# Kernel tuning notes

Hardware: AMD Instinct MI355X
Metric: run time of the kernel (lower is better)

## Reference

```python
import jax, jax.numpy as jnp
import numpy as np

B, NNB, D, FF, L = 128, 510, 128, 512, 3
N = NNB + 2  # 2 query tokens (first/last) + neighbors
SQRT_D = float(np.sqrt(D))
LOGIT_CLIP = 10.0
NINF = -1e9


def _layer_norm(x, g, b):
    m = jnp.mean(x, axis=-1, keepdims=True)
    v = jnp.var(x, axis=-1, keepdims=True)
    return (x - m) * jax.lax.rsqrt(v + 1e-5) * g + b


def _aafm(q, k, v, w):
    # Attention-free module: sigmoid(q) * (exp(w) @ (exp(k)*v)) / (exp(w) @ exp(k))
    w = w - jnp.max(w, axis=-1, keepdims=True)          # stable, cancels in ratio
    k = k - jnp.max(k, axis=1, keepdims=True)
    ew = jnp.exp(w)                                      # [B,N,N]
    ek = jnp.exp(k)                                      # [B,N,D]
    num = jnp.einsum('bts,bsd->btd', ew, ek * v)
    den = jnp.einsum('bts,bsd->btd', ew, ek)
    return jax.nn.sigmoid(q) * num / den


def setup_inputs() -> dict:
    key = jax.random.key(0)
    ks = jax.random.split(key, 32)
    s = 1.0 / np.sqrt(D)
    inp = {
        'lower_xy': jax.random.uniform(ks[0], (B, N, 2), jnp.float32),
        'load': jax.random.uniform(ks[1], (B,), jnp.float32) * 0.9 + 0.1,
        'lower_demand': jax.random.uniform(ks[2], (B, NNB, 1), jnp.float32) * 0.3,
        'lower_cur_ninf_mask': jnp.where(
            jax.random.uniform(ks[3], (B, 1, N)) < 0.1, NINF, 0.0).astype(jnp.float32),
        'lower_pairwise_dist': jax.random.uniform(ks[4], (B, N, N), jnp.float32),
        'neighbors_num_list': jnp.full((B,), NNB, dtype=jnp.int32),
        'lower_neighbors_index': jax.random.randint(ks[5], (B, NNB), 0, 100000),
        # learned params (torch Linear stored transposed: here [in, out], y = x @ W)
        'emb_W': jax.random.normal(ks[6], (2, D)) * s,
        'emb_b': jnp.zeros((D,), jnp.float32),
        'w_load': jax.random.normal(ks[7], (D,)) * s,
        'w_demand': jax.random.normal(ks[8], (D,)) * s,
        'Wq_first': jax.random.normal(ks[9], (D, D)) * s,
        'Wq_last': jax.random.normal(ks[10], (D, D)) * s,
        'alpha_com': jnp.ones((1,), jnp.float32),
        'Wq': jax.random.normal(ks[11], (L, D, D)) * s,
        'Wk': jax.random.normal(ks[12], (L, D, D)) * s,
        'Wv': jax.random.normal(ks[13], (L, D, D)) * s,
        'alpha_attn': jnp.ones((L,), jnp.float32),
        'ln1_g': jnp.ones((L, D), jnp.float32),
        'ln1_b': jnp.zeros((L, D), jnp.float32),
        'ln2_g': jnp.ones((L, D), jnp.float32),
        'ln2_b': jnp.zeros((L, D), jnp.float32),
        'ff_W1': jax.random.normal(ks[14], (L, D, FF)) * s,
        'ff_b1': jnp.zeros((L, FF), jnp.float32),
        'ff_W2': jax.random.normal(ks[15], (L, FF, D)) * (1.0 / np.sqrt(FF)),
        'ff_b2': jnp.zeros((L, D), jnp.float32),
    }
    return inp


def reference(lower_xy, load, lower_demand, lower_cur_ninf_mask, lower_pairwise_dist,
              neighbors_num_list, lower_neighbors_index,
              emb_W, emb_b, w_load, w_demand, Wq_first, Wq_last, alpha_com,
              Wq, Wk, Wv, alpha_attn, ln1_g, ln1_b, ln2_g, ln2_b,
              ff_W1, ff_b1, ff_W2, ff_b2):
    load3 = load[:, None, None]                           # [B,1,1]
    load3 = jnp.where(load3 == 0, 1.0, load3)
    fln = lower_xy @ emb_W + emb_b                        # [B,N,D]
    load_emb = load3 * w_load                             # [B,1,D]
    q_first = fln[:, 0:1] @ Wq_first + load_emb
    q_last = fln[:, 1:2] @ Wq_last + load_emb
    demand = jnp.clip(lower_demand / load3, 0.0, 1.0)     # [B,n,1]
    nb = fln[:, 2:] + demand * w_demand                   # [B,n,D]
    nb_mask = lower_cur_ninf_mask[:, 0, 2:]               # [B,n]
    nb = jnp.where((nb_mask < 0)[..., None], 0.0, nb)     # padding overwrite
    x = jnp.concatenate([q_first, q_last, nb], axis=1)    # [B,N,D]

    log_nb = jnp.log2(neighbors_num_list.astype(x.dtype))[:, None, None]
    spd = -log_nb * lower_pairwise_dist                   # [B,N,N]
    mask_full = jnp.broadcast_to(lower_cur_ninf_mask, spd.shape)

    for i in range(L):
        q = x @ Wq[i]; k = x @ Wk[i]; v = x @ Wv[i]
        aafm = _aafm(q, k, v, alpha_attn[i] * spd + mask_full)
        h = _layer_norm(x + aafm, ln1_g[i], ln1_b[i])
        ff = jax.nn.relu(h @ ff_W1[i] + ff_b1[i]) @ ff_W2[i] + ff_b2[i]
        x = _layer_norm(h + ff, ln2_g[i], ln2_b[i])

    q_out = x[:, 0:1] + x[:, 1:2]                         # [B,1,D]
    nbo = x[:, 2:]                                        # [B,n,D]
    bias_com = alpha_com * spd[:, 1, 2:][:, None, :]      # [B,1,n]
    score = jnp.einsum('bqd,bnd->bqn', q_out, nbo) / SQRT_D + bias_com
    score = LOGIT_CLIP * jnp.tanh(score) + lower_cur_ninf_mask[:, :, 2:]
    probs = jax.nn.softmax(score, axis=-1)[:, 0]          # [B,n]

    selected = jnp.argmax(probs, axis=-1)                 # greedy eval
    prob = jnp.take_along_axis(probs, selected[:, None], axis=-1)[:, 0]
    true_selected = jnp.take_along_axis(lower_neighbors_index, selected[:, None], axis=-1)[:, 0]
    return true_selected, prob
```

## Files before the change

### kernel.cpp

```cpp
#include <hip/hip_runtime.h>
#include <math.h>

constexpr int B   = 128;
constexpr int N   = 512;
constexpr int NNB = 510;
constexpr int D   = 128;
constexpr int FFH = 512;
constexpr int NL  = 3;

__device__ __forceinline__ float sigmoidf_(float x) { return 1.f / (1.f + expf(-x)); }

__device__ __forceinline__ float xla_fast_tanh(float x) {
    if (fabsf(x) < 0.0004f) return x;
    const float C = 7.99881172180175781f;
    float xc = fminf(fmaxf(x, -C), C);
    float x2 = __fmul_rn(xc, xc);
    float num = -2.76076847742355e-16f;
    num = __builtin_fmaf(x2, num, 2.00018790482477e-13f);
    num = __builtin_fmaf(x2, num, -8.60467152213735e-11f);
    num = __builtin_fmaf(x2, num, 5.12229709037114e-08f);
    num = __builtin_fmaf(x2, num, 1.48572235717979e-05f);
    num = __builtin_fmaf(x2, num, 6.37261928875436e-04f);
    num = __builtin_fmaf(x2, num, 4.89352455891786e-03f);
    num = __fmul_rn(xc, num);
    float den = 1.19825839466702e-06f;
    den = __builtin_fmaf(x2, den, 1.18534705686654e-04f);
    den = __builtin_fmaf(x2, den, 2.26843463243900e-03f);
    den = __builtin_fmaf(x2, den, 4.89352518554385e-03f);
    return num / den;
}

__global__ __launch_bounds__(128) void build_x_kernel(
    const float* __restrict__ xy, const float* __restrict__ load,
    const float* __restrict__ demand, const float* __restrict__ mask,
    const float* __restrict__ embW, const float* __restrict__ embb,
    const float* __restrict__ wload, const float* __restrict__ wdem,
    const float* __restrict__ Wqf, const float* __restrict__ Wql,
    float* __restrict__ x)
{
    __shared__ float fln[128];
    const int bn = blockIdx.x;
    const int b  = bn >> 9;
    const int n  = bn & 511;
    const int d  = threadIdx.x;
    float l = load[b];
    float load3 = (l == 0.f) ? 1.f : l;

    if (n >= 2) {
        const int j = n - 2;
        float m = mask[(size_t)b * N + n];
        float out = 0.f;
        if (!(m < 0.f)) {
            float x0 = xy[(size_t)bn * 2 + 0];
            float x1 = xy[(size_t)bn * 2 + 1];
            float fl = x0 * embW[d] + x1 * embW[D + d] + embb[d];
            float dm = demand[(size_t)b * NNB + j] / load3;
            dm = fminf(fmaxf(dm, 0.f), 1.f);
            out = fl + dm * wdem[d];
        }
        x[(size_t)bn * D + d] = out;
    } else {
        float x0 = xy[(size_t)bn * 2 + 0];
        float x1 = xy[(size_t)bn * 2 + 1];
        fln[d] = x0 * embW[d] + x1 * embW[D + d] + embb[d];
        __syncthreads();
        const float* W = (n == 0) ? Wqf : Wql;
        float acc = 0.f;
        #pragma unroll 8
        for (int e = 0; e < D; ++e) acc = fmaf(fln[e], W[(size_t)e * D + d], acc);
        x[(size_t)bn * D + d] = acc + load3 * wload[d];
    }
}

template<bool BIAS, bool RELU>
__global__ __launch_bounds__(256) void gemm_f32(
    const float* __restrict__ A, const float* __restrict__ W,
    const float* __restrict__ bias, float* __restrict__ C,
    int M, int K, int Nc)
{
    __shared__ float As[64][40];
    __shared__ float Ws[32][132];
    const int m0 = blockIdx.x * 64;
    const int n0 = blockIdx.y * 128;
    const int tid = threadIdx.x;
    const int tc = tid & 31;
    const int tr = tid >> 5;

    const int ar0 = tid >> 3,          ac0 = (tid & 7) * 4;
    const int ar1 = (tid + 256) >> 3,  ac1 = ((tid + 256) & 7) * 4;
    int wr[4], wc[4];
    #pragma unroll
    for (int i = 0; i < 4; ++i) {
        int f = tid + i * 256;
        wr[i] = f >> 5; wc[i] = (f & 31) * 4;
    }

    float4 acc[8];
    #pragma unroll
    for (int r = 0; r < 8; ++r) acc[r] = make_float4(0.f, 0.f, 0.f, 0.f);

    {
        float4 a0 = *(const float4*)&A[(size_t)(m0 + ar0) * K + ac0];
        float4 a1 = *(const float4*)&A[(size_t)(m0 + ar1) * K + ac1];
        float4 w0 = *(const float4*)&W[(size_t)(0 + wr[0]) * Nc + n0 + wc[0]];
        float4 w1 = *(const float4*)&W[(size_t)(0 + wr[1]) * Nc + n0 + wc[1]];
        float4 w2 = *(const float4*)&W[(size_t)(0 + wr[2]) * Nc + n0 + wc[2]];
        float4 w3 = *(const float4*)&W[(size_t)(0 + wr[3]) * Nc + n0 + wc[3]];
        *(float4*)&As[ar0][ac0] = a0;
        *(float4*)&As[ar1][ac1] = a1;
        *(float4*)&Ws[wr[0]][wc[0]] = w0;
        *(float4*)&Ws[wr[1]][wc[1]] = w1;
        *(float4*)&Ws[wr[2]][wc[2]] = w2;
        *(float4*)&Ws[wr[3]][wc[3]] = w3;
    }
    __syncthreads();

    for (int kt = 0; kt < K; kt += 32) {
        const bool more = (kt + 32) < K;
        float4 na0, na1, nw0, nw1, nw2, nw3;
        if (more) {
            int kn = kt + 32;
            na0 = *(const float4*)&A[(size_t)(m0 + ar0) * K + kn + ac0];
            na1 = *(const float4*)&A[(size_t)(m0 + ar1) * K + kn + ac1];
            nw0 = *(const float4*)&W[(size_t)(kn + wr[0]) * Nc + n0 + wc[0]];
            nw1 = *(const float4*)&W[(size_t)(kn + wr[1]) * Nc + n0 + wc[1]];
            nw2 = *(const float4*)&W[(size_t)(kn + wr[2]) * Nc + n0 + wc[2]];
            nw3 = *(const float4*)&W[(size_t)(kn + wr[3]) * Nc + n0 + wc[3]];
        }
        #pragma unroll
        for (int kk = 0; kk < 32; kk += 4) {
            float4 w0 = *(float4*)&Ws[kk + 0][tc * 4];
            float4 w1 = *(float4*)&Ws[kk + 1][tc * 4];
            float4 w2 = *(float4*)&Ws[kk + 2][tc * 4];
            float4 w3 = *(float4*)&Ws[kk + 3][tc * 4];
            #pragma unroll
            for (int r = 0; r < 8; ++r) {
                float4 a4 = *(float4*)&As[tr * 8 + r][kk];
                acc[r].x = fmaf(a4.x, w0.x, acc[r].x); acc[r].x = fmaf(a4.y, w1.x, acc[r].x);
                acc[r].x = fmaf(a4.z, w2.x, acc[r].x); acc[r].x = fmaf(a4.w, w3.x, acc[r].x);
                acc[r].y = fmaf(a4.x, w0.y, acc[r].y); acc[r].y = fmaf(a4.y, w1.y, acc[r].y);
                acc[r].y = fmaf(a4.z, w2.y, acc[r].y); acc[r].y = fmaf(a4.w, w3.y, acc[r].y);
                acc[r].z = fmaf(a4.x, w0.z, acc[r].z); acc[r].z = fmaf(a4.y, w1.z, acc[r].z);
                acc[r].z = fmaf(a4.z, w2.z, acc[r].z); acc[r].z = fmaf(a4.w, w3.z, acc[r].z);
                acc[r].w = fmaf(a4.x, w0.w, acc[r].w); acc[r].w = fmaf(a4.y, w1.w, acc[r].w);
                acc[r].w = fmaf(a4.z, w2.w, acc[r].w); acc[r].w = fmaf(a4.w, w3.w, acc[r].w);
            }
        }
        if (more) {
            __syncthreads();
            *(float4*)&As[ar0][ac0] = na0;
            *(float4*)&As[ar1][ac1] = na1;
            *(float4*)&Ws[wr[0]][wc[0]] = nw0;
            *(float4*)&Ws[wr[1]][wc[1]] = nw1;
            *(float4*)&Ws[wr[2]][wc[2]] = nw2;
            *(float4*)&Ws[wr[3]][wc[3]] = nw3;
            __syncthreads();
        }
    }

    float4 bv = make_float4(0.f, 0.f, 0.f, 0.f);
    if (BIAS) bv = *(const float4*)&bias[n0 + tc * 4];
    #pragma unroll
    for (int r = 0; r < 8; ++r) {
        float4 o = acc[r];
        if (BIAS) { o.x += bv.x; o.y += bv.y; o.z += bv.z; o.w += bv.w; }
        if (RELU) {
            o.x = fmaxf(o.x, 0.f); o.y = fmaxf(o.y, 0.f);
            o.z = fmaxf(o.z, 0.f); o.w = fmaxf(o.w, 0.f);
        }
        *(float4*)&C[(size_t)(m0 + tr * 8 + r) * Nc + n0 + tc * 4] = o;
    }
}

__global__ __launch_bounds__(128) void colmax_part(
    const float* __restrict__ k, float* __restrict__ part)
{
    int b = blockIdx.x >> 3, c = blockIdx.x & 7, d = threadIdx.x;
    const float* kp = k + ((size_t)b * N + c * 64) * D + d;
    float m = -3.4e38f;
    #pragma unroll 8
    for (int s = 0; s < 64; ++s) m = fmaxf(m, kp[(size_t)s * D]);
    part[(size_t)blockIdx.x * D + d] = m;
}

__global__ __launch_bounds__(128) void ekv_build(
    const float* __restrict__ k, const float* __restrict__ v,
    const float* __restrict__ part, float* __restrict__ ekv)
{
    int b = blockIdx.x >> 3, c = blockIdx.x & 7, d = threadIdx.x;
    float m = -3.4e38f;
    #pragma unroll
    for (int j = 0; j < 8; ++j) m = fmaxf(m, part[((size_t)b * 8 + j) * D + d]);
    for (int s = 0; s < 64; ++s) {
        int sg = c * 64 + s;
        size_t off = ((size_t)b * N + sg) * D + d;
        float ek = expf(k[off] - m);
        size_t o2 = ((size_t)b * N + sg) * 256;
        ekv[o2 + d]       = ek * v[off];
        ekv[o2 + 128 + d] = ek;
    }
}

__global__ __launch_bounds__(256) void attn_kernel(
    const float* __restrict__ pdist, const float* __restrict__ mask,
    const float* __restrict__ ekv, const float* __restrict__ q,
    const int* __restrict__ nnum, const float* __restrict__ alphaAttn, int layer,
    float* __restrict__ att)
{
    __shared__ float ew[16][516];
    __shared__ float red16[16][16];
    __shared__ float rmax[16];
    const int d0  = blockIdx.x;
    const int xcd = d0 & 7;
    const int idx = d0 >> 3;
    const int tl  = idx & 31;
    const int b   = (idx >> 5) * 8 + xcd;
    const int t0  = tl * 16;
    const int tid = threadIdx.x;
    const float la = -log2f((float)nnum[b]) * alphaAttn[layer];
    const float* pd = pdist + ((size_t)b * N + t0) * N;
    const float* mk = mask + (size_t)b * N;

    #pragma unroll
    for (int i = 0; i < 8; ++i) {
        int f = tid + i * 256;
        int r = f >> 7, s4 = (f & 127) * 4;
        float4 p = *(const float4*)&pd[(size_t)r * N + s4];
        float4 m = *(const float4*)&mk[s4];
        float4 w;
        w.x = fmaf(la, p.x, m.x); w.y = fmaf(la, p.y, m.y);
        w.z = fmaf(la, p.z, m.z); w.w = fmaf(la, p.w, m.w);
        *(float4*)&ew[r][s4] = w;
    }
    __syncthreads();
    {
        int r = tid >> 4, j0 = tid & 15;
        float m = -3.4e38f;
        #pragma unroll 8
        for (int j = 0; j < 32; ++j) m = fmaxf(m, ew[r][j0 + 16 * j]);
        red16[r][j0] = m;
    }
    __syncthreads();
    if (tid < 16) {
        float m = red16[tid][0];
        #pragma unroll
        for (int j = 1; j < 16; ++j) m = fmaxf(m, red16[tid][j]);
        rmax[tid] = m;
    }
    __syncthreads();
    #pragma unroll
    for (int i = 0; i < 8; ++i) {
        int f = tid + i * 256;
        int r = f >> 7, s4 = (f & 127) * 4;
        float m = rmax[r];
        float4 w = *(float4*)&ew[r][s4];
        w.x = expf(w.x - m); w.y = expf(w.y - m);
        w.z = expf(w.z - m); w.w = expf(w.w - m);
        *(float4*)&ew[r][s4] = w;
    }
    __syncthreads();

    const int lane = tid & 63;
    const int wv   = tid >> 6;
    const int c4   = lane * 4;
    float4 acc[4];
    #pragma unroll
    for (int r = 0; r < 4; ++r) acc[r] = make_float4(0.f, 0.f, 0.f, 0.f);
    const float* ep = ekv + (size_t)b * N * 256 + c4;
    float4 e0 = *(const float4*)&ep[0 * 256];
    float4 e1 = *(const float4*)&ep[1 * 256];
    float4 e2 = *(const float4*)&ep[2 * 256];
    float4 e3 = *(const float4*)&ep[3 * 256];
    for (int s = 0; s < N; s += 4) {
        float4 f0 = e0, f1 = e1, f2 = e2, f3 = e3;
        int sn = (s + 4 < N) ? (s + 4) : s;
        e0 = *(const float4*)&ep[(size_t)(sn + 0) * 256];
        e1 = *(const float4*)&ep[(size_t)(sn + 1) * 256];
        e2 = *(const float4*)&ep[(size_t)(sn + 2) * 256];
        e3 = *(const float4*)&ep[(size_t)(sn + 3) * 256];
        #pragma unroll
        for (int r = 0; r < 4; ++r) {
            float4 a = *(float4*)&ew[wv * 4 + r][s];
            acc[r].x = fmaf(a.x, f0.x, acc[r].x); acc[r].x = fmaf(a.y, f1.x, acc[r].x);
            acc[r].x = fmaf(a.z, f2.x, acc[r].x); acc[r].x = fmaf(a.w, f3.x, acc[r].x);
            acc[r].y = fmaf(a.x, f0.y, acc[r].y); acc[r].y = fmaf(a.y, f1.y, acc[r].y);
            acc[r].y = fmaf(a.z, f2.y, acc[r].y); acc[r].y = fmaf(a.w, f3.y, acc[r].y);
            acc[r].z = fmaf(a.x, f0.z, acc[r].z); acc[r].z = fmaf(a.y, f1.z, acc[r].z);
            acc[r].z = fmaf(a.z, f2.z, acc[r].z); acc[r].z = fmaf(a.w, f3.z, acc[r].z);
            acc[r].w = fmaf(a.x, f0.w, acc[r].w); acc[r].w = fmaf(a.y, f1.w, acc[r].w);
            acc[r].w = fmaf(a.z, f2.w, acc[r].w); acc[r].w = fmaf(a.w, f3.w, acc[r].w);
        }
    }
    __syncthreads();
    if (c4 >= 128) {
        #pragma unroll
        for (int r = 0; r < 4; ++r)
            *(float4*)&ew[wv * 4 + r][c4 - 128] = acc[r];
    }
    __syncthreads();
    if (c4 < 128) {
        #pragma unroll
        for (int r = 0; r < 4; ++r) {
            int row = wv * 4 + r;
            size_t off = ((size_t)b * N + t0 + row) * D + c4;
            float4 qq = *(const float4*)&q[off];
            float4 dd = *(float4*)&ew[row][c4];
            float4 o;
            o.x = sigmoidf_(qq.x) * acc[r].x / dd.x;
            o.y = sigmoidf_(qq.y) * acc[r].y / dd.y;
            o.z = sigmoidf_(qq.z) * acc[r].z / dd.z;
            o.w = sigmoidf_(qq.w) * acc[r].w / dd.w;
            *(float4*)&att[off] = o;
        }
    }
}

__global__ __launch_bounds__(256) void ln_kernel(
    const float* a, const float* b2, const float* g, const float* be, float* out)
{
    int w = threadIdx.x >> 6, lane = threadIdx.x & 63;
    size_t row = (size_t)blockIdx.x * 4 + w;
    size_t base = row * D + lane * 2;
    float2 av = *(const float2*)&a[base];
    float2 bv = *(const float2*)&b2[base];
    float x0 = av.x + bv.x, x1 = av.y + bv.y;
    float s = x0 + x1;
    #pragma unroll
    for (int off = 32; off > 0; off >>= 1) s += __shfl_xor(s, off);
    float mean = s * (1.f / 128.f);
    float d0 = x0 - mean, d1 = x1 - mean;
    float ss = d0 * d0 + d1 * d1;
    #pragma unroll
    for (int off = 32; off > 0; off >>= 1) ss += __shfl_xor(ss, off);
    float rs = rsqrtf(ss * (1.f / 128.f) + 1e-5f);
    float2 o;
    o.x = d0 * rs * g[lane * 2]     + be[lane * 2];
    o.y = d1 * rs * g[lane * 2 + 1] + be[lane * 2 + 1];
    *(float2*)&out[base] = o;
}

__global__ __launch_bounds__(512) void k_final(
    const float* __restrict__ x, const float* __restrict__ pdist,
    const float* __restrict__ mask, const int* __restrict__ nnum,
    const int* __restrict__ nidx, const float* __restrict__ aCom,
    float* __restrict__ out)
{
    __shared__ float  sc[512];
    __shared__ float  ee[512];
    __shared__ double qo[128];
    int b = blockIdx.x, tid = threadIdx.x;
    const float* xb = x + (size_t)b * N * D;
    if (tid < 128) qo[tid] = (double)xb[tid] + (double)xb[128 + tid];
    __syncthreads();
    if (tid < NNB) {
        const float* xr = xb + (size_t)(2 + tid) * 128;
        double s = 0.0;
        for (int dd = 0; dd < 128; ++dd) s += qo[dd] * (double)xr[dd];
        double lg = -log2((double)nnum[b]);
        s = s / 11.313708498984761
          + (double)aCom[0] * lg * (double)pdist[((size_t)b * 512 + 1) * 512 + 2 + tid];
        float t = xla_fast_tanh((float)s);
        sc[tid] = __fadd_rn(__fmul_rn(10.0f, t),
                            mask[(size_t)b * 512 + 2 + tid]);
    }
    __syncthreads();
    if (tid == 0) {
        float m = -3.4e38f;
        for (int n2 = 0; n2 < NNB; ++n2) m = fmaxf(m, sc[n2]);
        float S = 0.f;
        for (int n2 = 0; n2 < NNB; ++n2) {
            float e = expf(__fadd_rn(sc[n2], -m));
            ee[n2] = e;
            S = __fadd_rn(S, e);
        }
        float bestp = -1.f; int sel = 0;
        for (int n2 = 0; n2 < NNB; ++n2) {
            float p = ee[n2] / S;
            if (p > bestp) { bestp = p; sel = n2; }
        }
        out[b]     = (float)nidx[(size_t)b * NNB + sel];
        out[B + b] = bestp;
    }
}

extern "C" void kernel_launch(void* const* d_in, const int* in_sizes, int n_in,
                              void* d_out, int out_size, void* d_ws, size_t ws_size,
                              hipStream_t stream)
{
    const float* xy     = (const float*)d_in[0];
    const float* load   = (const float*)d_in[1];
    const float* demand = (const float*)d_in[2];
    const float* mask   = (const float*)d_in[3];
    const float* pdist  = (const float*)d_in[4];
    const int*   nnum   = (const int*)d_in[5];
    const int*   nidx   = (const int*)d_in[6];
    const float* embW   = (const float*)d_in[7];
    const float* embb   = (const float*)d_in[8];
    const float* wload  = (const float*)d_in[9];
    const float* wdem   = (const float*)d_in[10];
    const float* Wqf    = (const float*)d_in[11];
    const float* Wql    = (const float*)d_in[12];
    const float* aCom   = (const float*)d_in[13];
    const float* Wq     = (const float*)d_in[14];
    const float* Wk     = (const float*)d_in[15];
    const float* Wv     = (const float*)d_in[16];
    const float* aAttn  = (const float*)d_in[17];
    const float* ln1g   = (const float*)d_in[18];
    const float* ln1b   = (const float*)d_in[19];
    const float* ln2g   = (const float*)d_in[20];
    const float* ln2b   = (const float*)d_in[21];
    const float* fW1    = (const float*)d_in[22];
    const float* fb1    = (const float*)d_in[23];
    const float* fW2    = (const float*)d_in[24];
    const float* fb2    = (const float*)d_in[25];
    float* out = (float*)d_out;

    float* ws = (float*)d_ws;
    const size_t SZ = (size_t)B * N * D;
    float* xbuf = ws;
    float* qbuf = ws + SZ;
    float* kbuf = ws + 2 * SZ;
    float* vbuf = ws + 3 * SZ;
    float* ekv  = ws + 4 * SZ;
    float* part = qbuf;
    float* bigh = qbuf;
    float* aux  = vbuf;

    build_x_kernel<<<B * N, 128, 0, stream>>>(xy, load, demand, mask, embW, embb,
                                              wload, wdem, Wqf, Wql, xbuf);
    const int M  = B * N;
    const int MH = M / 2;
    for (int l = 0; l < NL; ++l) {
        dim3 g1(M / 64, 1);
        gemm_f32<false, false><<<g1, 256, 0, stream>>>(xbuf, Wk + (size_t)l * D * D, nullptr, kbuf, M, D, D);
        gemm_f32<false, false><<<g1, 256, 0, stream>>>(xbuf, Wv + (size_t)l * D * D, nullptr, vbuf, M, D, D);
        colmax_part<<<B * 8, 128, 0, stream>>>(kbuf, part);
        ekv_build<<<B * 8, 128, 0, stream>>>(kbuf, vbuf, part, ekv);
        gemm_f32<false, false><<<g1, 256, 0, stream>>>(xbuf, Wq + (size_t)l * D * D, nullptr, qbuf, M, D, D);
        attn_kernel<<<B * 32, 256, 0, stream>>>(pdist, mask, ekv, qbuf, nnum, aAttn, l, kbuf);
        ln_kernel<<<M / 4, 256, 0, stream>>>(xbuf, kbuf, ln1g + l * D, ln1b + l * D, xbuf);
        for (int h = 0; h < 2; ++h) {
            dim3 g2(MH / 64, FFH / 128);
            dim3 g3(MH / 64, 1);
            gemm_f32<true, true><<<g2, 256, 0, stream>>>(xbuf + (size_t)h * MH * D, fW1 + (size_t)l * D * FFH,
                                                         fb1 + l * FFH, bigh, MH, D, FFH);
            gemm_f32<true, false><<<g3, 256, 0, stream>>>(bigh, fW2 + (size_t)l * FFH * D,
                                                          fb2 + l * D, aux + (size_t)h * MH * D, MH, FFH, D);
        }
        ln_kernel<<<M / 4, 256, 0, stream>>>(xbuf, aux, ln2g + l * D, ln2b + l * D, xbuf);
    }
    k_final<<<B, 512, 0, stream>>>(xbuf, pdist, mask, nnum, nidx, aCom, out);
}
```

Before: 2.134 ms.

## Split AAFM matmul over the source dimension across waves with LDS reduction

The AAFM weighted-sum kernel now gives each of the four waves a quarter of the source tokens and all 16 target rows, instead of 4 rows over all 512 sources. Each ekv float4 load from global memory is then reused across 16 rows rather than 4, so global traffic per block drops by a factor of four. The cost is 64 accumulator registers per thread, which may lower occupancy, plus a tree reduction of partial sums through LDS with extra barriers. The final division by the denominator now uses lane shuffles.

```diff
diff --git a/kernel.cpp b/kernel.cpp
--- a/kernel.cpp
+++ b/kernel.cpp
@@ -9,6 +9,8 @@
 constexpr int NL  = 3;
 
 __device__ __forceinline__ float sigmoidf_(float x) { return 1.f / (1.f + expf(-x)); }
+
+#define F4ADD(a, b) { (a).x += (b).x; (a).y += (b).y; (a).z += (b).z; (a).w += (b).w; }
 
 __device__ __forceinline__ float xla_fast_tanh(float x) {
     if (fabsf(x) < 0.0004f) return x;
@@ -263,24 +265,26 @@
     const int lane = tid & 63;
     const int wv   = tid >> 6;
     const int c4   = lane * 4;
-    float4 acc[4];
-    #pragma unroll
-    for (int r = 0; r < 4; ++r) acc[r] = make_float4(0.f, 0.f, 0.f, 0.f);
+    float4 acc[16];
+    #pragma unroll
+    for (int r = 0; r < 16; ++r) acc[r] = make_float4(0.f, 0.f, 0.f, 0.f);
     const float* ep = ekv + (size_t)b * N * 256 + c4;
-    float4 e0 = *(const float4*)&ep[0 * 256];
-    float4 e1 = *(const float4*)&ep[1 * 256];
-    float4 e2 = *(const float4*)&ep[2 * 256];
-    float4 e3 = *(const float4*)&ep[3 * 256];
-    for (int s = 0; s < N; s += 4) {
+    const int sb = wv * 128;
+    float4 e0 = *(const float4*)&ep[(size_t)(sb + 0) * 256];
+    float4 e1 = *(const float4*)&ep[(size_t)(sb + 1) * 256];
+    float4 e2 = *(const float4*)&ep[(size_t)(sb + 2) * 256];
+    float4 e3 = *(const float4*)&ep[(size_t)(sb + 3) * 256];
+    for (int it = 0; it < 32; ++it) {
+        const int s = sb + it * 4;
         float4 f0 = e0, f1 = e1, f2 = e2, f3 = e3;
-        int sn = (s + 4 < N) ? (s + 4) : s;
+        int sn = (it < 31) ? (s + 4) : s;
         e0 = *(const float4*)&ep[(size_t)(sn + 0) * 256];
         e1 = *(const float4*)&ep[(size_t)(sn + 1) * 256];
         e2 = *(const float4*)&ep[(size_t)(sn + 2) * 256];
         e3 = *(const float4*)&ep[(size_t)(sn + 3) * 256];
         #pragma unroll
-        for (int r = 0; r < 4; ++r) {
-            float4 a = *(float4*)&ew[wv * 4 + r][s];
+        for (int r = 0; r < 16; ++r) {
+            float4 a = *(float4*)&ew[r][s];
             acc[r].x = fmaf(a.x, f0.x, acc[r].x); acc[r].x = fmaf(a.y, f1.x, acc[r].x);
             acc[r].x = fmaf(a.z, f2.x, acc[r].x); acc[r].x = fmaf(a.w, f3.x, acc[r].x);
             acc[r].y = fmaf(a.x, f0.y, acc[r].y); acc[r].y = fmaf(a.y, f1.y, acc[r].y);
@@ -291,26 +295,51 @@
             acc[r].w = fmaf(a.z, f2.w, acc[r].w); acc[r].w = fmaf(a.w, f3.w, acc[r].w);
         }
     }
-    __syncthreads();
-    if (c4 >= 128) {
-        #pragma unroll
-        for (int r = 0; r < 4; ++r)
-            *(float4*)&ew[wv * 4 + r][c4 - 128] = acc[r];
-    }
-    __syncthreads();
-    if (c4 < 128) {
-        #pragma unroll
-        for (int r = 0; r < 4; ++r) {
-            int row = wv * 4 + r;
-            size_t off = ((size_t)b * N + t0 + row) * D + c4;
-            float4 qq = *(const float4*)&q[off];
-            float4 dd = *(float4*)&ew[row][c4];
-            float4 o;
-            o.x = sigmoidf_(qq.x) * acc[r].x / dd.x;
-            o.y = sigmoidf_(qq.y) * acc[r].y / dd.y;
-            o.z = sigmoidf_(qq.z) * acc[r].z / dd.z;
-            o.w = sigmoidf_(qq.w) * acc[r].w / dd.w;
-            *(float4*)&att[off] = o;
+
+    float* red = &ew[0][0];
+    __syncthreads();
+    if (wv == 1) {
+        #pragma unroll
+        for (int r = 0; r < 16; ++r) *(float4*)&red[r * 256 + c4] = acc[r];
+    }
+    if (wv == 3) {
+        #pragma unroll
+        for (int r = 0; r < 16; ++r) *(float4*)&red[4096 + r * 256 + c4] = acc[r];
+    }
+    __syncthreads();
+    if (wv == 0) {
+        #pragma unroll
+        for (int r = 0; r < 16; ++r) { float4 t = *(float4*)&red[r * 256 + c4]; F4ADD(acc[r], t); }
+    }
+    if (wv == 2) {
+        #pragma unroll
+        for (int r = 0; r < 16; ++r) { float4 t = *(float4*)&red[4096 + r * 256 + c4]; F4ADD(acc[r], t); }
+    }
+    __syncthreads();
+    if (wv == 2) {
+        #pragma unroll
+        for (int r = 0; r < 16; ++r) *(float4*)&red[r * 256 + c4] = acc[r];
+    }
+    __syncthreads();
+    if (wv == 0) {
+        #pragma unroll
+        for (int r = 0; r < 16; ++r) { float4 t = *(float4*)&red[r * 256 + c4]; F4ADD(acc[r], t); }
+        #pragma unroll
+        for (int r = 0; r < 16; ++r) {
+            float dx = __shfl(acc[r].x, lane + 32);
+            float dy = __shfl(acc[r].y, lane + 32);
+            float dz = __shfl(acc[r].z, lane + 32);
+            float dw = __shfl(acc[r].w, lane + 32);
+            if (lane < 32) {
+                size_t off = ((size_t)b * N + t0 + r) * D + c4;
+                float4 qq = *(const float4*)&q[off];
+                float4 o;
+                o.x = sigmoidf_(qq.x) * acc[r].x / dx;
+                o.y = sigmoidf_(qq.y) * acc[r].y / dy;
+                o.z = sigmoidf_(qq.z) * acc[r].z / dz;
+                o.w = sigmoidf_(qq.w) * acc[r].w / dw;
+                *(float4*)&att[off] = o;
+            }
         }
     }
 }
```

Result: no change. 2.141 ms (+0.3%).
